# Optimization experiments

Measured on AMD Instinct MI355X. Metric: run time of the kernel, lower is better.

The kernel has to match this reference:

```python
import jax, jax.numpy as jnp
import numpy as np

N_EMBD = 768
N_HEAD = 12
DIM_HEAD = N_EMBD // N_HEAD


def setup_inputs() -> dict:
    key = jax.random.key(0)
    k1, k2, k3 = jax.random.split(key, 3)
    B, T = 4, 2048
    x = jax.random.normal(k1, (B, T, N_EMBD), dtype=jnp.float32)
    # torch Linear(n_embd, 3*n_embd, bias=False): y = x @ W.T, W:[3C,C].
    # Store pre-transposed [C,3C] for direct matmul.
    s = 1.0 / np.sqrt(N_EMBD)
    W_qkv = jax.random.uniform(k2, (N_EMBD, 3 * N_EMBD), dtype=jnp.float32, minval=-s, maxval=s)
    W_proj = jax.random.uniform(k3, (N_EMBD, N_EMBD), dtype=jnp.float32, minval=-s, maxval=s)
    return {"x": x, "W_qkv": W_qkv, "W_proj": W_proj}


def reference(x, W_qkv, W_proj):
    B, T, C = x.shape
    qkv = x @ W_qkv                                  # [B,T,3C]
    q, k, v = jnp.split(qkv, 3, axis=-1)
    def heads(t):  # [B,T,C] -> [B,H,T,Dh]
        return t.reshape(B, T, N_HEAD, DIM_HEAD).transpose(0, 2, 1, 3)
    q, k, v = heads(q), heads(k), heads(v)
    # Source divides by scale = dim_head**-0.5, i.e. multiplies by sqrt(dim_head).
    scores = jnp.einsum('bhtd,bhsd->bhts', q, k) * jnp.sqrt(jnp.float32(DIM_HEAD))
    attn = jax.nn.softmax(scores, axis=-1)           # [B,H,T,T] materialized
    y = jnp.einsum('bhts,bhsd->bhtd', attn, v)       # [B,H,T,Dh]
    y = y.transpose(0, 2, 1, 3).reshape(B, T, C)
    return y @ W_proj
```

## Files before the change

### kernel.cpp

```cpp
#include <hip/hip_runtime.h>

typedef _Float16 f16;
typedef f16 f16x4 __attribute__((ext_vector_type(4)));
typedef f16 f16x8 __attribute__((ext_vector_type(8)));
typedef __fp16 h16x2 __attribute__((ext_vector_type(2)));
typedef float floatx4 __attribute__((ext_vector_type(4)));

#define LDT 72
#define LDE 136
#define QSCALE 11.5415603271117f

__global__ __launch_bounds__(256) void transpose_f32_f16_tiled(const float* __restrict__ in,
                                                               f16* __restrict__ out,
                                                               int K, int N) {
  __shared__ f16 tile[64][LDT];
  int k0 = blockIdx.x * 64, n0 = blockIdx.y * 64;
  int tid = threadIdx.x;
  int r = tid >> 4, c4 = (tid & 15) * 4;
  for (int p = 0; p < 4; ++p) {
    int rr = r + p * 16;
    float4 v = *(const float4*)(in + (size_t)(k0 + rr) * N + n0 + c4);
    tile[c4 + 0][rr] = (f16)v.x;
    tile[c4 + 1][rr] = (f16)v.y;
    tile[c4 + 2][rr] = (f16)v.z;
    tile[c4 + 3][rr] = (f16)v.w;
  }
  __syncthreads();
  int rn = tid >> 3, ck = (tid & 7) * 8;
  for (int p = 0; p < 2; ++p) {
    int rr = rn + p * 32;
    *(uint4*)(out + (size_t)(n0 + rr) * K + k0 + ck) = *(const uint4*)(&tile[rr][ck]);
  }
}

__global__ __launch_bounds__(256) void gemm1_qkv(const float* __restrict__ A,
                                                 const f16* __restrict__ Bt,
                                                 f16* __restrict__ q16, f16* __restrict__ k16,
                                                 f16* __restrict__ vt) {
  __shared__ f16 smem[2 * 128 * LDT];
  f16* As = smem;
  f16* Bs = smem + 128 * LDT;
  int tid = threadIdx.x;
  int lane = tid & 63, wid = tid >> 6;
  int quad = lane >> 4, l16 = lane & 15;
  int wy = wid >> 1, wx = wid & 1;
  int m0 = blockIdx.x * 128, n0 = blockIdx.y * 128;
  int srow = tid >> 3, scol = (tid & 7) * 8;
  floatx4 acc[4][4] = {};
  for (int k0 = 0; k0 < 768; k0 += 64) {
    for (int p = 0; p < 4; ++p) {
      int r = srow + p * 32;
      const float* src = A + (size_t)(m0 + r) * 768 + k0 + scol;
      float4 v0 = *(const float4*)(src);
      float4 v1 = *(const float4*)(src + 4);
      f16x8 hv = {(f16)v0.x, (f16)v0.y, (f16)v0.z, (f16)v0.w,
                  (f16)v1.x, (f16)v1.y, (f16)v1.z, (f16)v1.w};
      *(f16x8*)(As + r * LDT + scol) = hv;
      *(uint4*)(Bs + r * LDT + scol) = *(const uint4*)(Bt + (size_t)(n0 + r) * 768 + k0 + scol);
    }
    __syncthreads();
    for (int kk = 0; kk < 64; kk += 32) {
      f16x8 af[4], bfr[4];
      for (int i = 0; i < 4; ++i)
        af[i] = *(const f16x8*)(As + (wy * 64 + i * 16 + l16) * LDT + kk + quad * 8);
      for (int j = 0; j < 4; ++j)
        bfr[j] = *(const f16x8*)(Bs + (wx * 64 + j * 16 + l16) * LDT + kk + quad * 8);
      for (int i = 0; i < 4; ++i)
        for (int j = 0; j < 4; ++j)
          acc[i][j] = __builtin_amdgcn_mfma_f32_16x16x32_f16(af[i], bfr[j], acc[i][j], 0, 0, 0);
    }
    __syncthreads();
  }
  int b = m0 >> 11, t0 = m0 & 2047;
  if (n0 < 1536) {
    for (int i = 0; i < 4; ++i)
      for (int j = 0; j < 4; ++j)
        for (int r = 0; r < 4; ++r) {
          int t = t0 + wy * 64 + i * 16 + quad * 4 + r;
          int col = n0 + wx * 64 + j * 16 + l16;
          float a = acc[i][j][r];
          if (col < 768) {
            int h = col >> 6, d = col & 63;
            q16[((size_t)(b * 12 + h)) * 131072 + (size_t)t * 64 + d] = (f16)(a * QSCALE);
          } else {
            int c = col - 768;
            int h = c >> 6, d = c & 63;
            k16[((size_t)(b * 12 + h)) * 131072 + (size_t)t * 64 + d] = (f16)a;
          }
        }
  } else {
    f16* Vtile = smem;
    int h0 = (n0 - 1536) >> 6;
    for (int i = 0; i < 4; ++i)
      for (int j = 0; j < 4; ++j) {
        int cl = wx * 64 + j * 16 + l16;
        int rl = wy * 64 + i * 16 + quad * 4;
        for (int r = 0; r < 4; ++r)
          Vtile[cl * LDE + rl + r] = (f16)acc[i][j][r];
      }
    __syncthreads();
    int u = tid & 15;
    for (int p = 0; p < 8; ++p) {
      int c = (tid >> 4) + p * 16;
      *(uint4*)(vt + ((size_t)(b * 12 + h0 + (c >> 6))) * 131072 +
                (size_t)(c & 63) * 2048 + t0 + u * 8) =
          *(const uint4*)(Vtile + c * LDE + u * 8);
    }
  }
}

__global__ __launch_bounds__(256) void gemm_bt_f16(const f16* __restrict__ A,
                                                   const f16* __restrict__ Bt,
                                                   float* __restrict__ C,
                                                   int M, int N, int K) {
  __shared__ f16 As[128 * LDT];
  __shared__ f16 Bs[128 * LDT];
  int tid = threadIdx.x;
  int lane = tid & 63, wid = tid >> 6;
  int quad = lane >> 4, l16 = lane & 15;
  int wy = wid >> 1, wx = wid & 1;
  int m0 = blockIdx.x * 128, n0 = blockIdx.y * 128;
  int srow = tid >> 3, scol = (tid & 7) * 8;
  floatx4 acc[4][4] = {};
  for (int k0 = 0; k0 < K; k0 += 64) {
    for (int p = 0; p < 4; ++p) {
      int r = srow + p * 32;
      *(uint4*)(As + r * LDT + scol) = *(const uint4*)(A + (size_t)(m0 + r) * K + k0 + scol);
      *(uint4*)(Bs + r * LDT + scol) = *(const uint4*)(Bt + (size_t)(n0 + r) * K + k0 + scol);
    }
    __syncthreads();
    for (int kk = 0; kk < 64; kk += 32) {
      f16x8 af[4], bfr[4];
      for (int i = 0; i < 4; ++i)
        af[i] = *(const f16x8*)(As + (wy * 64 + i * 16 + l16) * LDT + kk + quad * 8);
      for (int j = 0; j < 4; ++j)
        bfr[j] = *(const f16x8*)(Bs + (wx * 64 + j * 16 + l16) * LDT + kk + quad * 8);
      for (int i = 0; i < 4; ++i)
        for (int j = 0; j < 4; ++j)
          acc[i][j] = __builtin_amdgcn_mfma_f32_16x16x32_f16(af[i], bfr[j], acc[i][j], 0, 0, 0);
    }
    __syncthreads();
  }
  for (int i = 0; i < 4; ++i) {
    int row = m0 + wy * 64 + i * 16 + quad * 4;
    for (int j = 0; j < 4; ++j) {
      int col = n0 + wx * 64 + j * 16 + l16;
      for (int r = 0; r < 4; ++r)
        C[(size_t)(row + r) * N + col] = acc[i][j][r];
    }
  }
}

__global__ __launch_bounds__(512, 1) void flash_attn(const f16* __restrict__ q16,
                                                     const f16* __restrict__ k16,
                                                     const f16* __restrict__ vT,
                                                     f16* __restrict__ y) {
  __shared__ f16 Ks[128 * 64];
  __shared__ f16 Vt[64 * 128];
  const int T = 2048;
  int xcd = blockIdx.x & 7, yb = blockIdx.x >> 3;
  int bh = xcd * 6 + (yb >> 4);
  int qt = yb & 15;
  int b = bh / 12, h = bh - b * 12;
  int tid = threadIdx.x;
  int lane = tid & 63, wid = tid >> 6;
  int quad = lane >> 4, l16 = lane & 15;
  int rk = tid >> 3, kch = tid & 7;
  int rv = tid >> 4, vch = tid & 15;
  int kswz = (kch ^ (rk & 7)) * 8;
  int vswz = (vch ^ (rv & 15)) * 8;
  size_t hb = (size_t)bh * T * 64;

  f16x8 qf[2];
  {
    size_t qrow = hb + (size_t)(qt * 128 + wid * 16 + l16) * 64 + quad * 8;
    qf[0] = *(const f16x8*)(q16 + qrow);
    qf[1] = *(const f16x8*)(q16 + qrow + 32);
  }
  f16x4 ones4;
  for (int e = 0; e < 4; ++e) ones4[e] = (f16)1.0f;

  float m_i = -1e30f, l_i = 0.f;
  floatx4 o[4] = {};

  for (int kt = 0; kt < 16; ++kt) {
    if (kt) __syncthreads();
    for (int p = 0; p < 2; ++p) {
      int r = rk + p * 64;
      *(uint4*)(Ks + r * 64 + kswz) =
          *(const uint4*)(k16 + hb + (size_t)(kt * 128 + r) * 64 + kch * 8);
      int d = rv + p * 32;
      *(uint4*)(Vt + d * 128 + vswz) =
          *(const uint4*)(vT + hb + (size_t)d * T + kt * 128 + vch * 8);
    }
    __syncthreads();

    floatx4 sf[8];
    const floatx4 z4 = {0.f, 0.f, 0.f, 0.f};
    for (int i = 0; i < 8; ++i) sf[i] = z4;
    for (int kk = 0; kk < 2; ++kk)
      for (int i = 0; i < 8; ++i) {
        int row = i * 16 + l16;
        f16x8 kf = *(const f16x8*)(Ks + row * 64 + (((kk * 4 + quad) ^ (l16 & 7)) * 8));
        sf[i] = __builtin_amdgcn_mfma_f32_16x16x32_f16(kf, qf[kk], sf[i], 0, 0, 0);
      }

    float mx = fmaxf(fmaxf(sf[0][0], sf[0][1]), fmaxf(sf[0][2], sf[0][3]));
    for (int i = 1; i < 8; ++i)
      mx = fmaxf(mx, fmaxf(fmaxf(sf[i][0], sf[i][1]), fmaxf(sf[i][2], sf[i][3])));
    mx = fmaxf(mx, __shfl_xor(mx, 16));
    mx = fmaxf(mx, __shfl_xor(mx, 32));
    float m_new = fmaxf(m_i, mx);
    float alpha = exp2f(m_i - m_new);
    m_i = m_new;
    for (int i = 0; i < 4; ++i) o[i] *= alpha;

    f16x4 pf[8];
    for (int i = 0; i < 8; ++i) {
      union { h16x2 h; f16 f[2]; } a2, b2;
      a2.h = __builtin_amdgcn_cvt_pkrtz(sf[i][0] - m_new, sf[i][1] - m_new);
      b2.h = __builtin_amdgcn_cvt_pkrtz(sf[i][2] - m_new, sf[i][3] - m_new);
      f16x4 uu = {a2.f[0], a2.f[1], b2.f[0], b2.f[1]};
#if __has_builtin(__builtin_elementwise_exp2)
      pf[i] = __builtin_elementwise_exp2(uu);
#else
      for (int r = 0; r < 4; ++r) pf[i][r] = (f16)exp2f((float)uu[r]);
#endif
    }

    floatx4 rs = z4;
    for (int si = 0; si < 8; ++si)
      rs = __builtin_amdgcn_mfma_f32_16x16x16f16(ones4, pf[si], rs, 0, 0, 0);
    l_i = l_i * alpha + rs[0];

    for (int i = 0; i < 4; ++i)
      for (int si = 0; si < 8; ++si) {
        int d = i * 16 + l16;
        int cch = si * 2 + (quad >> 1);
        f16x4 vf = *(const f16x4*)(Vt + d * 128 + ((cch ^ l16) * 8) + (quad & 1) * 4);
        o[i] = __builtin_amdgcn_mfma_f32_16x16x16f16(vf, pf[si], o[i], 0, 0, 0);
      }
  }

  float invl = 1.0f / l_i;
  int t = qt * 128 + wid * 16 + l16;
  size_t off = ((size_t)(b * T + t)) * 768 + h * 64;
  for (int i = 0; i < 4; ++i)
    for (int r = 0; r < 4; ++r)
      y[off + i * 16 + quad * 4 + r] = (f16)(o[i][r] * invl);
}

extern "C" void kernel_launch(void* const* d_in, const int* in_sizes, int n_in,
                              void* d_out, int out_size, void* d_ws, size_t ws_size,
                              hipStream_t stream) {
  const float* x     = (const float*)d_in[0];
  const float* Wqkv  = (const float*)d_in[1];
  const float* Wproj = (const float*)d_in[2];
  float* out = (float*)d_out;
  char* ws = (char*)d_ws;
  f16* q16    = (f16*)ws;
  f16* k16    = (f16*)(ws + 12582912);
  f16* vT16   = (f16*)(ws + 25165824);
  f16* y16    = (f16*)(ws + 37748736);
  f16* WqkvT  = (f16*)(ws + 50331648);
  f16* WprojT = (f16*)(ws + 53870592);

  transpose_f32_f16_tiled<<<dim3(12, 36), 256, 0, stream>>>(Wqkv, WqkvT, 768, 2304);
  transpose_f32_f16_tiled<<<dim3(12, 12), 256, 0, stream>>>(Wproj, WprojT, 768, 768);
  gemm1_qkv<<<dim3(64, 18), 256, 0, stream>>>(x, WqkvT, q16, k16, vT16);
  flash_attn<<<768, 512, 0, stream>>>(q16, k16, vT16, y16);
  gemm_bt_f16<<<dim3(64, 6), 256, 0, stream>>>(y16, WprojT, out, 8192, 768, 768);
}
```

Baseline: 242.6 us.

## Pre-convert x to fp16 and stage GEMM tiles via direct global-to-LDS loads

Adds a separate kernel that converts x to fp16 up front, reusing the y16 workspace buffer. Both GEMM kernels now load their A and B tiles straight into LDS with global_load_lds instead of going through registers. This removes the conversion and register round-trip from the GEMM inner loop and lets the loads bypass VGPRs. In exchange the LDS layout becomes unpadded (stride 64), so the fragment reads may hit bank conflicts, and there is an extra pass over x in memory.

```diff
diff --git a/kernel.cpp b/kernel.cpp
--- a/kernel.cpp
+++ b/kernel.cpp
@@ -9,6 +9,22 @@
 #define LDT 72
 #define LDE 136
 #define QSCALE 11.5415603271117f
+
+__device__ __forceinline__ void gld16(const void* g, void* l) {
+  __builtin_amdgcn_global_load_lds((const __attribute__((address_space(1))) unsigned int*)g,
+                                   (__attribute__((address_space(3))) unsigned int*)l,
+                                   16, 0, 0);
+}
+
+__global__ __launch_bounds__(256) void cvt_f32_f16(const float* __restrict__ in,
+                                                   f16* __restrict__ out) {
+  size_t i = ((size_t)blockIdx.x * 256 + threadIdx.x) * 8;
+  float4 v0 = *(const float4*)(in + i);
+  float4 v1 = *(const float4*)(in + i + 4);
+  f16x8 h = {(f16)v0.x, (f16)v0.y, (f16)v0.z, (f16)v0.w,
+             (f16)v1.x, (f16)v1.y, (f16)v1.z, (f16)v1.w};
+  *(f16x8*)(out + i) = h;
+}
 
 __global__ __launch_bounds__(256) void transpose_f32_f16_tiled(const float* __restrict__ in,
                                                                f16* __restrict__ out,
@@ -33,38 +49,34 @@
   }
 }
 
-__global__ __launch_bounds__(256) void gemm1_qkv(const float* __restrict__ A,
+__global__ __launch_bounds__(256) void gemm1_qkv(const f16* __restrict__ A,
                                                  const f16* __restrict__ Bt,
                                                  f16* __restrict__ q16, f16* __restrict__ k16,
                                                  f16* __restrict__ vt) {
-  __shared__ f16 smem[2 * 128 * LDT];
+  __shared__ f16 smem[17408];
   f16* As = smem;
-  f16* Bs = smem + 128 * LDT;
+  f16* Bs = smem + 8192;
   int tid = threadIdx.x;
   int lane = tid & 63, wid = tid >> 6;
   int quad = lane >> 4, l16 = lane & 15;
   int wy = wid >> 1, wx = wid & 1;
   int m0 = blockIdx.x * 128, n0 = blockIdx.y * 128;
-  int srow = tid >> 3, scol = (tid & 7) * 8;
+  int gr = lane >> 3, gc = (lane & 7) * 8;
   floatx4 acc[4][4] = {};
   for (int k0 = 0; k0 < 768; k0 += 64) {
     for (int p = 0; p < 4; ++p) {
-      int r = srow + p * 32;
-      const float* src = A + (size_t)(m0 + r) * 768 + k0 + scol;
-      float4 v0 = *(const float4*)(src);
-      float4 v1 = *(const float4*)(src + 4);
-      f16x8 hv = {(f16)v0.x, (f16)v0.y, (f16)v0.z, (f16)v0.w,
-                  (f16)v1.x, (f16)v1.y, (f16)v1.z, (f16)v1.w};
-      *(f16x8*)(As + r * LDT + scol) = hv;
-      *(uint4*)(Bs + r * LDT + scol) = *(const uint4*)(Bt + (size_t)(n0 + r) * 768 + k0 + scol);
+      int c = wid * 4 + p;
+      int row = c * 8 + gr;
+      gld16(A + (size_t)(m0 + row) * 768 + k0 + gc, As + c * 512);
+      gld16(Bt + (size_t)(n0 + row) * 768 + k0 + gc, Bs + c * 512);
     }
     __syncthreads();
     for (int kk = 0; kk < 64; kk += 32) {
       f16x8 af[4], bfr[4];
       for (int i = 0; i < 4; ++i)
-        af[i] = *(const f16x8*)(As + (wy * 64 + i * 16 + l16) * LDT + kk + quad * 8);
+        af[i] = *(const f16x8*)(As + (wy * 64 + i * 16 + l16) * 64 + kk + quad * 8);
       for (int j = 0; j < 4; ++j)
-        bfr[j] = *(const f16x8*)(Bs + (wx * 64 + j * 16 + l16) * LDT + kk + quad * 8);
+        bfr[j] = *(const f16x8*)(Bs + (wx * 64 + j * 16 + l16) * 64 + kk + quad * 8);
       for (int i = 0; i < 4; ++i)
         for (int j = 0; j < 4; ++j)
           acc[i][j] = __builtin_amdgcn_mfma_f32_16x16x32_f16(af[i], bfr[j], acc[i][j], 0, 0, 0);
@@ -113,28 +125,29 @@
                                                    const f16* __restrict__ Bt,
                                                    float* __restrict__ C,
                                                    int M, int N, int K) {
-  __shared__ f16 As[128 * LDT];
-  __shared__ f16 Bs[128 * LDT];
+  __shared__ f16 As[8192];
+  __shared__ f16 Bs[8192];
   int tid = threadIdx.x;
   int lane = tid & 63, wid = tid >> 6;
   int quad = lane >> 4, l16 = lane & 15;
   int wy = wid >> 1, wx = wid & 1;
   int m0 = blockIdx.x * 128, n0 = blockIdx.y * 128;
-  int srow = tid >> 3, scol = (tid & 7) * 8;
+  int gr = lane >> 3, gc = (lane & 7) * 8;
   floatx4 acc[4][4] = {};
   for (int k0 = 0; k0 < K; k0 += 64) {
     for (int p = 0; p < 4; ++p) {
-      int r = srow + p * 32;
-      *(uint4*)(As + r * LDT + scol) = *(const uint4*)(A + (size_t)(m0 + r) * K + k0 + scol);
-      *(uint4*)(Bs + r * LDT + scol) = *(const uint4*)(Bt + (size_t)(n0 + r) * K + k0 + scol);
+      int c = wid * 4 + p;
+      int row = c * 8 + gr;
+      gld16(A + (size_t)(m0 + row) * K + k0 + gc, As + c * 512);
+      gld16(Bt + (size_t)(n0 + row) * K + k0 + gc, Bs + c * 512);
     }
     __syncthreads();
     for (int kk = 0; kk < 64; kk += 32) {
       f16x8 af[4], bfr[4];
       for (int i = 0; i < 4; ++i)
-        af[i] = *(const f16x8*)(As + (wy * 64 + i * 16 + l16) * LDT + kk + quad * 8);
+        af[i] = *(const f16x8*)(As + (wy * 64 + i * 16 + l16) * 64 + kk + quad * 8);
       for (int j = 0; j < 4; ++j)
-        bfr[j] = *(const f16x8*)(Bs + (wx * 64 + j * 16 + l16) * LDT + kk + quad * 8);
+        bfr[j] = *(const f16x8*)(Bs + (wx * 64 + j * 16 + l16) * 64 + kk + quad * 8);
       for (int i = 0; i < 4; ++i)
         for (int j = 0; j < 4; ++j)
           acc[i][j] = __builtin_amdgcn_mfma_f32_16x16x32_f16(af[i], bfr[j], acc[i][j], 0, 0, 0);
@@ -264,10 +277,12 @@
   f16* y16    = (f16*)(ws + 37748736);
   f16* WqkvT  = (f16*)(ws + 50331648);
   f16* WprojT = (f16*)(ws + 53870592);
-
+  f16* x16 = y16;
+
+  cvt_f32_f16<<<3072, 256, 0, stream>>>(x, x16);
   transpose_f32_f16_tiled<<<dim3(12, 36), 256, 0, stream>>>(Wqkv, WqkvT, 768, 2304);
   transpose_f32_f16_tiled<<<dim3(12, 12), 256, 0, stream>>>(Wproj, WprojT, 768, 768);
-  gemm1_qkv<<<dim3(64, 18), 256, 0, stream>>>(x, WqkvT, q16, k16, vT16);
+  gemm1_qkv<<<dim3(64, 18), 256, 0, stream>>>(x16, WqkvT, q16, k16, vT16);
   flash_attn<<<768, 512, 0, stream>>>(q16, k16, vT16, y16);
   gemm_bt_f16<<<dim3(64, 6), 256, 0, stream>>>(y16, WprojT, out, 8192, 768, 768);
 }
```

Measured after the change: 250.8 us. 1.03x slower.
